# Optimization experiments

Hardware: AMD Instinct MI355X
Metric: run time of the kernel (lower is better)

The kernel has to match this reference:

```python
import jax, jax.numpy as jnp
import numpy as np

N = 100000   # total nodes
E = 1600000  # total edges
B = 256      # graphs per batch
F_NODE, F_EDGE, H = 35, 10, 64
N_CONV = 3
IN_DIM = 2 * H + F_EDGE  # 138
EPS = 1e-5


def setup_inputs() -> dict:
    key = jax.random.key(0)
    ks = jax.random.split(key, 16)
    node_features = jax.random.normal(ks[0], (N, F_NODE), dtype=jnp.float32)
    edge_index = jax.random.randint(ks[1], (2, E), 0, N, dtype=jnp.int64)
    edge_features = jax.random.uniform(ks[2], (E, F_EDGE), dtype=jnp.float32)
    graph_index = jnp.sort(jax.random.randint(ks[3], (N,), 0, B, dtype=jnp.int64))
    s = lambda fan_in: 1.0 / np.sqrt(fan_in)
    embed_w = jax.random.uniform(ks[4], (F_NODE, H), jnp.float32, -s(F_NODE), s(F_NODE))
    embed_b = jax.random.uniform(ks[5], (H,), jnp.float32, -s(F_NODE), s(F_NODE))
    gate_w = jax.random.uniform(ks[6], (N_CONV, IN_DIM, H), jnp.float32, -s(IN_DIM), s(IN_DIM))
    gate_b = jax.random.uniform(ks[7], (N_CONV, H), jnp.float32, -s(IN_DIM), s(IN_DIM))
    cand_w = jax.random.uniform(ks[8], (N_CONV, IN_DIM, H), jnp.float32, -s(IN_DIM), s(IN_DIM))
    cand_b = jax.random.uniform(ks[9], (N_CONV, H), jnp.float32, -s(IN_DIM), s(IN_DIM))
    bn_g = jnp.ones((N_CONV, H), dtype=jnp.float32)
    bn_b = jnp.zeros((N_CONV, H), dtype=jnp.float32)
    mlp_w1 = jax.random.uniform(ks[10], (H, 128), jnp.float32, -s(H), s(H))
    mlp_b1 = jax.random.uniform(ks[11], (128,), jnp.float32, -s(H), s(H))
    mlp_w2 = jax.random.uniform(ks[12], (128, 64), jnp.float32, -s(128), s(128))
    mlp_b2 = jax.random.uniform(ks[13], (64,), jnp.float32, -s(128), s(128))
    mlp_w3 = jax.random.uniform(ks[14], (64, 1), jnp.float32, -s(64), s(64))
    mlp_b3 = jax.random.uniform(ks[15], (1,), jnp.float32, -s(64), s(64))
    return dict(node_features=node_features, edge_index=edge_index,
                edge_features=edge_features, graph_index=graph_index,
                embed_w=embed_w, embed_b=embed_b,
                gate_w=gate_w, gate_b=gate_b, cand_w=cand_w, cand_b=cand_b,
                bn_g=bn_g, bn_b=bn_b,
                mlp_w1=mlp_w1, mlp_b1=mlp_b1, mlp_w2=mlp_w2, mlp_b2=mlp_b2,
                mlp_w3=mlp_w3, mlp_b3=mlp_b3)


def _conv(h, src, dst, edge_feat, gw, gb, cw, cb, gamma, beta):
    # gather -> concat -> gated message
    z = jnp.concatenate([h[src], h[dst], edge_feat], axis=1)  # [E, 2H+F_edge]
    g = jax.nn.sigmoid(z @ gw + gb)
    c = jax.nn.softplus(z @ cw + cb)
    m = g * c
    # scatter-add onto source nodes
    agg = jax.ops.segment_sum(m, src, num_segments=h.shape[0])
    # BatchNorm1d (training-mode batch stats, biased variance)
    mu = agg.mean(axis=0)
    var = agg.var(axis=0)
    agg_bn = (agg - mu) * jax.lax.rsqrt(var + EPS) * gamma + beta
    return jax.nn.softplus(h + agg_bn)


def reference(node_features, edge_index, edge_features, graph_index,
              embed_w, embed_b, gate_w, gate_b, cand_w, cand_b, bn_g, bn_b,
              mlp_w1, mlp_b1, mlp_w2, mlp_b2, mlp_w3, mlp_b3):
    src, dst = edge_index[0], edge_index[1]
    h = node_features @ embed_w + embed_b  # [N, H]
    for i in range(N_CONV):
        h = _conv(h, src, dst, edge_features,
                  gate_w[i], gate_b[i], cand_w[i], cand_b[i], bn_g[i], bn_b[i])
    # mean pool per graph (B is static = 256)
    pooled = jax.ops.segment_sum(h, graph_index, num_segments=B)
    counts = jax.ops.segment_sum(jnp.ones((h.shape[0],), h.dtype), graph_index, num_segments=B)
    pooled = pooled / jnp.clip(counts, 1.0, None)[:, None]
    x = jax.nn.softplus(pooled @ mlp_w1 + mlp_b1)
    x = jax.nn.softplus(x @ mlp_w2 + mlp_b2)
    return (x @ mlp_w3 + mlp_b3)[:, 0]  # [B]
```

## Files before the change

### kernel.cpp

```cpp
#include <hip/hip_runtime.h>
#include <hip/hip_bf16.h>

#define NN 100000
#define EE 1600000
#define BB 256
#define F_NODE 35
#define F_EDGE 10
#define HH 64
#define IN_DIM 138
#define N_CONV 3
#define EPSBN 1e-5f
#define NB1 ((NN + 255) / 256)

#define NWAVES 2000
#define NGROUPS 50
#define SUBLEN 200
#define EPW 800
#define EFSTR 12

typedef _Float16 half8 __attribute__((ext_vector_type(8)));
typedef float floatx4 __attribute__((ext_vector_type(4)));

__device__ __forceinline__ float softplus_fast(float x) {
    return fmaxf(x, 0.0f) + __logf(1.0f + __expf(-fabsf(x)));
}
__device__ __forceinline__ float sigmoid_fast(float x) {
    return __builtin_amdgcn_rcpf(1.0f + __expf(-x));
}

__global__ __launch_bounds__(256)
void hist_rank_kernel(const int* __restrict__ src, int* __restrict__ cnt,
                      int* __restrict__ rank) {
    int e = blockIdx.x * 256 + threadIdx.x;
    rank[e] = atomicAdd(&cnt[src[e]], 1);
}

__global__ __launch_bounds__(256)
void scan1_kernel(int* __restrict__ cnt, int* __restrict__ bsum, int n) {
    __shared__ int ls[256];
    int t = threadIdx.x;
    int i = blockIdx.x * 256 + t;
    int v = (i < n) ? cnt[i] : 0;
    ls[t] = v;
    __syncthreads();
#pragma unroll
    for (int off = 1; off < 256; off <<= 1) {
        int add = (t >= off) ? ls[t - off] : 0;
        __syncthreads();
        ls[t] += add;
        __syncthreads();
    }
    if (i < n) cnt[i] = ls[t] - v;
    if (t == 255) bsum[blockIdx.x] = ls[255];
}

__global__ __launch_bounds__(512)
void scan2_kernel(int* __restrict__ bsum, int nb) {
    __shared__ int ls[512];
    int t = threadIdx.x;
    int v = (t < nb) ? bsum[t] : 0;
    ls[t] = v;
    __syncthreads();
#pragma unroll
    for (int off = 1; off < 512; off <<= 1) {
        int add = (t >= off) ? ls[t - off] : 0;
        __syncthreads();
        ls[t] += add;
        __syncthreads();
    }
    if (t < nb) bsum[t] = ls[t] - v;
}

__global__ __launch_bounds__(256)
void scan3_kernel(int* __restrict__ cnt, const int* __restrict__ bsum, int n) {
    int i = blockIdx.x * 256 + threadIdx.x;
    if (i < n) cnt[i] += bsum[blockIdx.x];
}

__global__ __launch_bounds__(256)
void perm_kernel(const int* __restrict__ src, const int* __restrict__ rank,
                 const int* __restrict__ offs, int* __restrict__ perm) {
    int e = blockIdx.x * 256 + threadIdx.x;
    perm[offs[src[e]] + rank[e]] = e;
}

__global__ __launch_bounds__(256)
void gather_kernel(const int* __restrict__ perm,
                   const int* __restrict__ src, const int* __restrict__ dst,
                   const float* __restrict__ ef,
                   int* __restrict__ ssorted, int* __restrict__ dsorted,
                   _Float16* __restrict__ ef16) {
    int pos = blockIdx.x * 256 + threadIdx.x;
    int e = perm[pos];
    ssorted[pos] = src[e];
    dsorted[pos] = dst[e];
    const float2* efe = (const float2*)(ef + (size_t)e * F_EDGE);
    uint* op = (uint*)(ef16 + (size_t)pos * EFSTR);
#pragma unroll
    for (int i = 0; i < 5; i++) {
        float2 v = efe[i];
        _Float16 h0 = (_Float16)v.x;
        _Float16 h1 = (_Float16)v.y;
        op[i] = (uint)*(unsigned short*)&h0 | ((uint)*(unsigned short*)&h1 << 16);
    }
    op[5] = 0u;
}

__global__ __launch_bounds__(256)
void prep_w_kernel(const float* __restrict__ gw, const float* __restrict__ cw,
                   _Float16* __restrict__ wT) {
    int idx = blockIdx.x * 256 + threadIdx.x;
    if (idx >= 3 * 128 * 160) return;
    int k = idx % 160;
    int n = (idx / 160) & 127;
    int layer = idx / (160 * 128);
    float v = 0.f;
    if (k < IN_DIM)
        v = (n < 64) ? gw[layer * IN_DIM * HH + k * HH + n]
                     : cw[layer * IN_DIM * HH + k * HH + (n - 64)];
    wT[idx] = (_Float16)v;
}

__global__ __launch_bounds__(256)
void embed_kernel(const float* __restrict__ nf, const float* __restrict__ w,
                  const float* __restrict__ bias, float* __restrict__ h,
                  _Float16* __restrict__ h16, int n) {
    __shared__ float wl[F_NODE * HH];
    int tid = threadIdx.x;
    for (int i = tid; i < F_NODE * HH; i += 256) wl[i] = w[i];
    __syncthreads();
    int idx = blockIdx.x * 256 + tid;
    int node = idx >> 6, j = idx & 63;
    if (node >= n) return;
    float acc = bias[j];
    const float* row = nf + node * F_NODE;
#pragma unroll
    for (int k = 0; k < F_NODE; k++) acc += row[k] * wl[k * HH + j];
    h[idx] = acc;
    h16[idx] = (_Float16)acc;
}

__device__ __forceinline__ void load_A(const _Float16* __restrict__ h16,
                                       const _Float16* __restrict__ ef16,
                                       int s, int d, int eg, int quad,
                                       uint4& A0, uint4& A1, uint4& A2, uint4& A3,
                                       uint4& A4) {
    const uint4* hs = (const uint4*)(h16 + (size_t)s * HH);
    const uint4* hd = (const uint4*)(h16 + (size_t)d * HH);
    A0 = hs[quad];
    A1 = hs[quad + 4];
    A2 = hd[quad];
    A3 = hd[quad + 4];
    uint4 z; z.x = z.y = z.z = z.w = 0u;
    A4 = z;
    const _Float16* p = ef16 + (size_t)eg * EFSTR;
    if (quad == 0) {
        uint2 a = *(const uint2*)p;
        uint2 b = *(const uint2*)(p + 4);
        A4.x = a.x; A4.y = a.y; A4.z = b.x; A4.w = b.y;
    } else if (quad == 1) {
        uint2 a = *(const uint2*)(p + 8);
        A4.x = a.x; A4.y = a.y;
    }
}

__global__ __launch_bounds__(64, 2)
void edge_conv_mfma(const _Float16* __restrict__ h16,
                    const int* __restrict__ esrc,
                    const int* __restrict__ edst,
                    const _Float16* __restrict__ ef16,
                    const _Float16* __restrict__ wT,
                    const float* __restrict__ gb, const float* __restrict__ cb,
                    float* __restrict__ agg) {
    int lane = threadIdx.x;
    int quad = lane >> 4, n15 = lane & 15;
    int base = blockIdx.x * EPW + ((n15 >> 2) * SUBLEN) + (n15 & 3);

    half8 B[8][5];
#pragma unroll
    for (int t = 0; t < 8; t++) {
        const _Float16* wr = wT + (t * 16 + n15) * 160 + quad * 8;
#pragma unroll
        for (int ks = 0; ks < 5; ks++)
            B[t][ks] = *(const half8*)(wr + ks * 32);
    }
    float gb0 = gb[n15], gb1 = gb[16 + n15], gb2 = gb[32 + n15], gb3 = gb[48 + n15];
    float cb0 = cb[n15], cb1 = cb[16 + n15], cb2 = cb[32 + n15], cb3 = cb[48 + n15];

    int sprev = -1;
    float am0 = 0.f, am1 = 0.f, am2 = 0.f, am3 = 0.f;

    int eg = base;
    int s = esrc[eg], d = edst[eg];
    uint4 A0, A1, A2, A3, A4;
    load_A(h16, ef16, s, d, eg, quad, A0, A1, A2, A3, A4);
    int egn = base + 4;
    int sn = esrc[egn], dn = edst[egn];

    for (int g = 0; g < NGROUPS; g++) {
        int s_cur = s;

        floatx4 acc[8];
#pragma unroll
        for (int t = 0; t < 8; t++) acc[t] = (floatx4){0.f, 0.f, 0.f, 0.f};

        half8 a0 = __builtin_bit_cast(half8, A0);
        half8 a1 = __builtin_bit_cast(half8, A1);
        half8 a2 = __builtin_bit_cast(half8, A2);
        half8 a3 = __builtin_bit_cast(half8, A3);
        half8 a4 = __builtin_bit_cast(half8, A4);
#pragma unroll
        for (int t = 0; t < 8; t++) acc[t] = __builtin_amdgcn_mfma_f32_16x16x32_f16(a0, B[t][0], acc[t], 0, 0, 0);
#pragma unroll
        for (int t = 0; t < 8; t++) acc[t] = __builtin_amdgcn_mfma_f32_16x16x32_f16(a1, B[t][1], acc[t], 0, 0, 0);
#pragma unroll
        for (int t = 0; t < 8; t++) acc[t] = __builtin_amdgcn_mfma_f32_16x16x32_f16(a2, B[t][2], acc[t], 0, 0, 0);
#pragma unroll
        for (int t = 0; t < 8; t++) acc[t] = __builtin_amdgcn_mfma_f32_16x16x32_f16(a3, B[t][3], acc[t], 0, 0, 0);
#pragma unroll
        for (int t = 0; t < 8; t++) acc[t] = __builtin_amdgcn_mfma_f32_16x16x32_f16(a4, B[t][4], acc[t], 0, 0, 0);

        int egc = base + ((g + 1 < NGROUPS) ? (g + 1) * 4 : g * 4);
        load_A(h16, ef16, sn, dn, egc, quad, A0, A1, A2, A3, A4);
        s = sn; d = dn;
        int eg2 = base + ((g + 2 < NGROUPS) ? (g + 2) * 4 : (NGROUPS - 1) * 4);
        sn = esrc[eg2]; dn = edst[eg2];

#pragma unroll
        for (int r = 0; r < 4; r++) {
            int sr = __shfl(s_cur, quad * 4 + r, 64);
            if (sr != sprev) {
                if (sprev >= 0) {
                    float* p = agg + (size_t)sprev * HH + n15;
                    atomicAdd(p, am0);
                    atomicAdd(p + 16, am1);
                    atomicAdd(p + 32, am2);
                    atomicAdd(p + 48, am3);
                }
                sprev = sr;
                am0 = am1 = am2 = am3 = 0.f;
            }
            am0 += sigmoid_fast(acc[0][r] + gb0) * softplus_fast(acc[4][r] + cb0);
            am1 += sigmoid_fast(acc[1][r] + gb1) * softplus_fast(acc[5][r] + cb1);
            am2 += sigmoid_fast(acc[2][r] + gb2) * softplus_fast(acc[6][r] + cb2);
            am3 += sigmoid_fast(acc[3][r] + gb3) * softplus_fast(acc[7][r] + cb3);
        }
    }
    if (sprev >= 0) {
        float* p = agg + (size_t)sprev * HH + n15;
        atomicAdd(p, am0);
        atomicAdd(p + 16, am1);
        atomicAdd(p + 32, am2);
        atomicAdd(p + 48, am3);
    }
}

__global__ __launch_bounds__(256)
void bn_stats_kernel(const float* __restrict__ agg, float* __restrict__ stats, int total) {
    __shared__ float ls[256], lss[256];
    int tid = threadIdx.x;
    float s = 0.f, ss = 0.f;
    for (int idx = blockIdx.x * 256 + tid; idx < total; idx += gridDim.x * 256) {
        float v = agg[idx];
        s += v;
        ss += v * v;
    }
    ls[tid] = s;
    lss[tid] = ss;
    __syncthreads();
    if (tid < 64) {
        s = ls[tid] + ls[tid + 64] + ls[tid + 128] + ls[tid + 192];
        ss = lss[tid] + lss[tid + 64] + lss[tid + 128] + lss[tid + 192];
        atomicAdd(&stats[tid], s);
        atomicAdd(&stats[64 + tid], ss);
    }
}

__global__ __launch_bounds__(256)
void bn_update_kernel(float* __restrict__ h, _Float16* __restrict__ h16,
                      float* __restrict__ agg,
                      const float* __restrict__ stats,
                      const float* __restrict__ g, const float* __restrict__ b,
                      int total, float invN) {
    int idx = blockIdx.x * 256 + threadIdx.x;
    if (idx >= total) return;
    int j = idx & 63;
    float mu = stats[j] * invN;
    float var = stats[64 + j] * invN - mu * mu;
    var = fmaxf(var, 0.0f);
    float scale = g[j] * rsqrtf(var + EPSBN);
    float a = agg[idx];
    agg[idx] = 0.f;
    float v = h[idx] + (a - mu) * scale + b[j];
    float hv = softplus_fast(v);
    h[idx] = hv;
    h16[idx] = (_Float16)hv;
}

__global__ __launch_bounds__(256)
void pool_kernel(const float* __restrict__ h, const int* __restrict__ gi,
                 float* __restrict__ pool, float* __restrict__ counts, int n) {
    int tid = threadIdx.x;
    int grp = tid >> 6;
    int j = tid & 63;
    int n0 = blockIdx.x * 64 + grp * 16;
    if (n0 >= n) return;
    int nend = n0 + 16; if (nend > n) nend = n;
    int gprev = gi[n0];
    float a = 0.f;
    int cnt = 0;
    for (int nn = n0; nn < nend; nn++) {
        int gg = gi[nn];
        if (gg != gprev) {
            atomicAdd(&pool[gprev * 64 + j], a);
            if (j == 0) atomicAdd(&counts[gprev], (float)cnt);
            a = 0.f; cnt = 0; gprev = gg;
        }
        a += h[(size_t)nn * 64 + j];
        cnt++;
    }
    atomicAdd(&pool[gprev * 64 + j], a);
    if (j == 0) atomicAdd(&counts[gprev], (float)cnt);
}

__global__ __launch_bounds__(128)
void mlp_kernel(const float* __restrict__ pool, const float* __restrict__ counts,
                const float* __restrict__ w1, const float* __restrict__ b1,
                const float* __restrict__ w2, const float* __restrict__ b2,
                const float* __restrict__ w3, const float* __restrict__ b3,
                float* __restrict__ out) {
    __shared__ float x0[64], x1[128], x2[64];
    int b = blockIdx.x, t = threadIdx.x;
    if (t < 64) {
        float c = counts[b];
        c = c < 1.f ? 1.f : c;
        x0[t] = pool[b * 64 + t] / c;
    }
    __syncthreads();
    {
        float acc = 0.f;
#pragma unroll
        for (int k = 0; k < 64; k++) acc += x0[k] * w1[k * 128 + t];
        x1[t] = softplus_fast(acc + b1[t]);
    }
    __syncthreads();
    if (t < 64) {
        float acc = 0.f;
#pragma unroll
        for (int k = 0; k < 128; k++) acc += x1[k] * w2[k * 64 + t];
        x2[t] = softplus_fast(acc + b2[t]);
    }
    __syncthreads();
    if (t == 0) {
        float acc = 0.f;
        for (int k = 0; k < 64; k++) acc += x2[k] * w3[k];
        out[b] = acc + b3[0];
    }
}

extern "C" void kernel_launch(void* const* d_in, const int* in_sizes, int n_in,
                              void* d_out, int out_size, void* d_ws, size_t ws_size,
                              hipStream_t stream) {
    const float* nf      = (const float*)d_in[0];
    const int*   ei      = (const int*)d_in[1];
    const float* ef      = (const float*)d_in[2];
    const int*   gi      = (const int*)d_in[3];
    const float* embed_w = (const float*)d_in[4];
    const float* embed_b = (const float*)d_in[5];
    const float* gate_w  = (const float*)d_in[6];
    const float* gate_b  = (const float*)d_in[7];
    const float* cand_w  = (const float*)d_in[8];
    const float* cand_b  = (const float*)d_in[9];
    const float* bn_g    = (const float*)d_in[10];
    const float* bn_b    = (const float*)d_in[11];
    const float* w1      = (const float*)d_in[12];
    const float* b1      = (const float*)d_in[13];
    const float* w2      = (const float*)d_in[14];
    const float* b2      = (const float*)d_in[15];
    const float* w3      = (const float*)d_in[16];
    const float* b3      = (const float*)d_in[17];
    float* out = (float*)d_out;

    const int NH = NN * HH;
    char* p = (char*)d_ws;
    int*       offs    = (int*)p;              p += (size_t)NN * 4;
    float*     agg     = (float*)p;            p += (size_t)NH * 4;
    float*     stats   = (float*)p;            p += 3 * 128 * 4;
    float*     pool    = (float*)p;            p += (size_t)BB * HH * 4;
    float*     counts  = (float*)p;            p += (size_t)BB * 4;
    size_t zero_bytes = (size_t)(p - (char*)d_ws);
    float*     h       = (float*)p;            p += (size_t)NH * 4;
    _Float16*  h16     = (_Float16*)p;         p += (size_t)NH * 2;
    int*       ssorted = (int*)p;              p += (size_t)EE * 4;
    int*       dsorted = (int*)p;              p += (size_t)EE * 4;
    _Float16*  ef16    = (_Float16*)p;         p += (size_t)EE * EFSTR * 2;
    int*       perm    = (int*)p;              p += (size_t)EE * 4;
    int*       rank    = (int*)p;              p += (size_t)EE * 4;
    _Float16*  wTall   = (_Float16*)p;         p += (size_t)3 * 128 * 160 * 2;
    int*       bsum    = (int*)p;              p += 512 * 4;

    const int* src = ei;
    const int* dst = ei + EE;

    hipMemsetAsync(d_ws, 0, zero_bytes, stream);

    hist_rank_kernel<<<EE / 256, 256, 0, stream>>>(src, offs, rank);
    prep_w_kernel<<<(3 * 128 * 160 + 255) / 256, 256, 0, stream>>>(gate_w, cand_w, wTall);
    scan1_kernel<<<NB1, 256, 0, stream>>>(offs, bsum, NN);
    scan2_kernel<<<1, 512, 0, stream>>>(bsum, NB1);
    scan3_kernel<<<NB1, 256, 0, stream>>>(offs, bsum, NN);
    perm_kernel<<<EE / 256, 256, 0, stream>>>(src, rank, offs, perm);
    gather_kernel<<<EE / 256, 256, 0, stream>>>(perm, src, dst, ef, ssorted, dsorted, ef16);

    embed_kernel<<<NH / 256, 256, 0, stream>>>(nf, embed_w, embed_b, h, h16, NN);

    for (int i = 0; i < N_CONV; i++) {
        edge_conv_mfma<<<NWAVES, 64, 0, stream>>>(
            h16, ssorted, dsorted, ef16,
            wTall + (size_t)i * 128 * 160,
            gate_b + i * HH, cand_b + i * HH, agg);
        bn_stats_kernel<<<512, 256, 0, stream>>>(agg, stats + i * 128, NH);
        bn_update_kernel<<<NH / 256, 256, 0, stream>>>(
            h, h16, agg, stats + i * 128, bn_g + i * HH, bn_b + i * HH, NH, 1.0f / (float)NN);
    }

    pool_kernel<<<(NN + 63) / 64, 256, 0, stream>>>(h, gi, pool, counts, NN);
    mlp_kernel<<<BB, 128, 0, stream>>>(pool, counts, w1, b1, w2, b2, w3, b3, out);
}
```

Before: 895.0 us.

## Split edge conv output columns across two waves and fold scan3 into perm

The edge convolution kernel now runs two waves per block. Each wave computes half of the 64 output columns (two gate and two candidate tiles) over the same 400 edges, so per-wave weight registers and accumulators are halved and occupancy can rise, with 4000 blocks instead of 2000 single-wave ones. The cost is that every edge's gathered A rows are loaded twice, once per wave. Separately, the scan3 kernel is removed and perm_kernel adds the block prefix sum directly when computing offsets, saving one launch and one pass over the offsets array.

```diff
diff --git a/kernel.cpp b/kernel.cpp
--- a/kernel.cpp
+++ b/kernel.cpp
@@ -12,10 +12,10 @@
 #define EPSBN 1e-5f
 #define NB1 ((NN + 255) / 256)
 
-#define NWAVES 2000
-#define NGROUPS 50
-#define SUBLEN 200
-#define EPW 800
+#define NBLK 4000
+#define NGROUPS 25
+#define SUBLEN 100
+#define EPB 400
 #define EFSTR 12
 
 typedef _Float16 half8 __attribute__((ext_vector_type(8)));
@@ -72,16 +72,12 @@
 }
 
 __global__ __launch_bounds__(256)
-void scan3_kernel(int* __restrict__ cnt, const int* __restrict__ bsum, int n) {
-    int i = blockIdx.x * 256 + threadIdx.x;
-    if (i < n) cnt[i] += bsum[blockIdx.x];
-}
-
-__global__ __launch_bounds__(256)
 void perm_kernel(const int* __restrict__ src, const int* __restrict__ rank,
-                 const int* __restrict__ offs, int* __restrict__ perm) {
+                 const int* __restrict__ offs, const int* __restrict__ bsum,
+                 int* __restrict__ perm) {
     int e = blockIdx.x * 256 + threadIdx.x;
-    perm[offs[src[e]] + rank[e]] = e;
+    int s = src[e];
+    perm[offs[s] + bsum[s >> 8] + rank[e]] = e;
 }
 
 __global__ __launch_bounds__(256)
@@ -164,7 +160,7 @@
     }
 }
 
-__global__ __launch_bounds__(64, 2)
+__global__ __launch_bounds__(128, 3)
 void edge_conv_mfma(const _Float16* __restrict__ h16,
                     const int* __restrict__ esrc,
                     const int* __restrict__ edst,
@@ -172,23 +168,29 @@
                     const _Float16* __restrict__ wT,
                     const float* __restrict__ gb, const float* __restrict__ cb,
                     float* __restrict__ agg) {
-    int lane = threadIdx.x;
+    int lane = threadIdx.x & 63;
+    int w = threadIdx.x >> 6;
     int quad = lane >> 4, n15 = lane & 15;
-    int base = blockIdx.x * EPW + ((n15 >> 2) * SUBLEN) + (n15 & 3);
-
-    half8 B[8][5];
-#pragma unroll
-    for (int t = 0; t < 8; t++) {
-        const _Float16* wr = wT + (t * 16 + n15) * 160 + quad * 8;
-#pragma unroll
-        for (int ks = 0; ks < 5; ks++)
-            B[t][ks] = *(const half8*)(wr + ks * 32);
-    }
-    float gb0 = gb[n15], gb1 = gb[16 + n15], gb2 = gb[32 + n15], gb3 = gb[48 + n15];
-    float cb0 = cb[n15], cb1 = cb[16 + n15], cb2 = cb[32 + n15], cb3 = cb[48 + n15];
+    int base = blockIdx.x * EPB + ((n15 >> 2) * SUBLEN) + (n15 & 3);
+
+    int tg = 2 * w;
+    half8 B[4][5];
+#pragma unroll
+    for (int j = 0; j < 2; j++) {
+        const _Float16* wrg = wT + ((tg + j) * 16 + n15) * 160 + quad * 8;
+        const _Float16* wrc = wT + ((4 + tg + j) * 16 + n15) * 160 + quad * 8;
+#pragma unroll
+        for (int ks = 0; ks < 5; ks++) {
+            B[j][ks]     = *(const half8*)(wrg + ks * 32);
+            B[2 + j][ks] = *(const half8*)(wrc + ks * 32);
+        }
+    }
+    float gb0 = gb[tg * 16 + n15], gb1 = gb[(tg + 1) * 16 + n15];
+    float cb0 = cb[tg * 16 + n15], cb1 = cb[(tg + 1) * 16 + n15];
+    int colbase = tg * 16 + n15;
 
     int sprev = -1;
-    float am0 = 0.f, am1 = 0.f, am2 = 0.f, am3 = 0.f;
+    float am0 = 0.f, am1 = 0.f;
 
     int eg = base;
     int s = esrc[eg], d = edst[eg];
@@ -200,9 +202,9 @@
     for (int g = 0; g < NGROUPS; g++) {
         int s_cur = s;
 
-        floatx4 acc[8];
-#pragma unroll
-        for (int t = 0; t < 8; t++) acc[t] = (floatx4){0.f, 0.f, 0.f, 0.f};
+        floatx4 acc[4];
+#pragma unroll
+        for (int t = 0; t < 4; t++) acc[t] = (floatx4){0.f, 0.f, 0.f, 0.f};
 
         half8 a0 = __builtin_bit_cast(half8, A0);
         half8 a1 = __builtin_bit_cast(half8, A1);
@@ -210,15 +212,15 @@
         half8 a3 = __builtin_bit_cast(half8, A3);
         half8 a4 = __builtin_bit_cast(half8, A4);
 #pragma unroll
-        for (int t = 0; t < 8; t++) acc[t] = __builtin_amdgcn_mfma_f32_16x16x32_f16(a0, B[t][0], acc[t], 0, 0, 0);
-#pragma unroll
-        for (int t = 0; t < 8; t++) acc[t] = __builtin_amdgcn_mfma_f32_16x16x32_f16(a1, B[t][1], acc[t], 0, 0, 0);
-#pragma unroll
-        for (int t = 0; t < 8; t++) acc[t] = __builtin_amdgcn_mfma_f32_16x16x32_f16(a2, B[t][2], acc[t], 0, 0, 0);
-#pragma unroll
-        for (int t = 0; t < 8; t++) acc[t] = __builtin_amdgcn_mfma_f32_16x16x32_f16(a3, B[t][3], acc[t], 0, 0, 0);
-#pragma unroll
-        for (int t = 0; t < 8; t++) acc[t] = __builtin_amdgcn_mfma_f32_16x16x32_f16(a4, B[t][4], acc[t], 0, 0, 0);
+        for (int t = 0; t < 4; t++) acc[t] = __builtin_amdgcn_mfma_f32_16x16x32_f16(a0, B[t][0], acc[t], 0, 0, 0);
+#pragma unroll
+        for (int t = 0; t < 4; t++) acc[t] = __builtin_amdgcn_mfma_f32_16x16x32_f16(a1, B[t][1], acc[t], 0, 0, 0);
+#pragma unroll
+        for (int t = 0; t < 4; t++) acc[t] = __builtin_amdgcn_mfma_f32_16x16x32_f16(a2, B[t][2], acc[t], 0, 0, 0);
+#pragma unroll
+        for (int t = 0; t < 4; t++) acc[t] = __builtin_amdgcn_mfma_f32_16x16x32_f16(a3, B[t][3], acc[t], 0, 0, 0);
+#pragma unroll
+        for (int t = 0; t < 4; t++) acc[t] = __builtin_amdgcn_mfma_f32_16x16x32_f16(a4, B[t][4], acc[t], 0, 0, 0);
 
         int egc = base + ((g + 1 < NGROUPS) ? (g + 1) * 4 : g * 4);
         load_A(h16, ef16, sn, dn, egc, quad, A0, A1, A2, A3, A4);
@@ -231,27 +233,21 @@
             int sr = __shfl(s_cur, quad * 4 + r, 64);
             if (sr != sprev) {
                 if (sprev >= 0) {
-                    float* p = agg + (size_t)sprev * HH + n15;
+                    float* p = agg + (size_t)sprev * HH + colbase;
                     atomicAdd(p, am0);
                     atomicAdd(p + 16, am1);
-                    atomicAdd(p + 32, am2);
-                    atomicAdd(p + 48, am3);
                 }
                 sprev = sr;
-                am0 = am1 = am2 = am3 = 0.f;
+                am0 = am1 = 0.f;
             }
-            am0 += sigmoid_fast(acc[0][r] + gb0) * softplus_fast(acc[4][r] + cb0);
-            am1 += sigmoid_fast(acc[1][r] + gb1) * softplus_fast(acc[5][r] + cb1);
-            am2 += sigmoid_fast(acc[2][r] + gb2) * softplus_fast(acc[6][r] + cb2);
-            am3 += sigmoid_fast(acc[3][r] + gb3) * softplus_fast(acc[7][r] + cb3);
+            am0 += sigmoid_fast(acc[0][r] + gb0) * softplus_fast(acc[2][r] + cb0);
+            am1 += sigmoid_fast(acc[1][r] + gb1) * softplus_fast(acc[3][r] + cb1);
         }
     }
     if (sprev >= 0) {
-        float* p = agg + (size_t)sprev * HH + n15;
+        float* p = agg + (size_t)sprev * HH + colbase;
         atomicAdd(p, am0);
         atomicAdd(p + 16, am1);
-        atomicAdd(p + 32, am2);
-        atomicAdd(p + 48, am3);
     }
 }
 
@@ -408,14 +404,13 @@
     prep_w_kernel<<<(3 * 128 * 160 + 255) / 256, 256, 0, stream>>>(gate_w, cand_w, wTall);
     scan1_kernel<<<NB1, 256, 0, stream>>>(offs, bsum, NN);
     scan2_kernel<<<1, 512, 0, stream>>>(bsum, NB1);
-    scan3_kernel<<<NB1, 256, 0, stream>>>(offs, bsum, NN);
-    perm_kernel<<<EE / 256, 256, 0, stream>>>(src, rank, offs, perm);
+    perm_kernel<<<EE / 256, 256, 0, stream>>>(src, rank, offs, bsum, perm);
     gather_kernel<<<EE / 256, 256, 0, stream>>>(perm, src, dst, ef, ssorted, dsorted, ef16);
 
     embed_kernel<<<NH / 256, 256, 0, stream>>>(nf, embed_w, embed_b, h, h16, NN);
 
     for (int i = 0; i < N_CONV; i++) {
-        edge_conv_mfma<<<NWAVES, 64, 0, stream>>>(
+        edge_conv_mfma<<<NBLK, 128, 0, stream>>>(
             h16, ssorted, dsorted, ef16,
             wTall + (size_t)i * 128 * 160,
             gate_b + i * HH, cand_b + i * HH, agg);
```

Result: no change. 883.0 us (-1.3%).
